# Performance work log

Measured on AMD Instinct MI355X. Metric: run time of the kernel, lower is better.

The kernel has to match this reference:

```python
import jax, jax.numpy as jnp
import numpy as np
import math

B, S, D = 16, 2048, 64


def setup_inputs() -> dict:
    key = jax.random.key(0)
    k1, k2, k3 = jax.random.split(key, 3)
    Q = jax.random.normal(k1, (B, S, D), dtype=jnp.float32)
    K = jax.random.normal(k2, (B, S, D), dtype=jnp.float32)
    V = jax.random.normal(k3, (B, S, D), dtype=jnp.float32)
    # causal mask: True where attention is disallowed (strict upper triangle)
    mask = jnp.triu(jnp.ones((S, S), dtype=bool), k=1)
    mask = jnp.broadcast_to(mask, (B, S, S))
    return {"Q": Q, "K": K, "V": V, "mask": mask, "dk": 64}


def reference(Q, K, V, mask, dk):
    # w = Q K^T / sqrt(dk), masked fill with -1e8
    w = jnp.einsum("bqd,bkd->bqk", Q, K) / math.sqrt(dk)
    w = jnp.where(mask, jnp.float32(-1.0e8), w)
    # distance_func in the original returns 0 (constant, under no_grad),
    # so exp(-1e8 * 0) * w == w; output is softmax of masked scaled scores.
    distance_score = jnp.float32(0.0)
    s = jnp.exp(jnp.float32(-1.0e8) * distance_score) * w
    a = jax.nn.softmax(s, axis=-1)
    return a
```

## Files before the change

kernel.cpp:

```cpp
#include <hip/hip_runtime.h>

using bf16x8 = __attribute__((ext_vector_type(8))) short;
using u16x8  = __attribute__((ext_vector_type(8))) unsigned short;
using f32x4  = __attribute__((ext_vector_type(4))) float;

static constexpr int S  = 2048;
static constexpr int D  = 64;
static constexpr int TQ = 64;
static constexpr float QSCALE = 0.18033688f;

__device__ __forceinline__ unsigned short bf16_rne(float x) {
    unsigned u = __builtin_bit_cast(unsigned, x);
    u += 0x7FFFu + ((u >> 16) & 1u);
    return (unsigned short)(u >> 16);
}
__device__ __forceinline__ f32x4 mfma16(bf16x8 a, bf16x8 b, f32x4 c) {
    return __builtin_amdgcn_mfma_f32_16x16x32_bf16(a, b, c, 0, 0, 0);
}
__device__ __forceinline__ void lbar() {
    asm volatile("s_waitcnt lgkmcnt(0)" ::: "memory");
    __builtin_amdgcn_s_barrier();
    asm volatile("" ::: "memory");
}

__global__ __launch_bounds__(512, 1)
void monotonic_attn(const float* __restrict__ Qg, const float* __restrict__ Kg,
                    float* __restrict__ out)
{
    __shared__ unsigned short qlds[4096];
    __shared__ unsigned short kls[8][2][1024];
    __shared__ float red[8][64];

    const int bid  = blockIdx.x;
    const int wid  = (bid & 7) * ((int)gridDim.x >> 3) + (bid >> 3);
    const int b    = wid >> 4;
    const int pair = wid & 15;

    const int tid = threadIdx.x, lane = tid & 63, wv = tid >> 6;
    const int l15 = lane & 15, g = lane >> 4;

    const float* __restrict__ Qb = Qg + (size_t)b * S * D;
    const float* __restrict__ Kb = Kg + (size_t)b * S * D;
    float* __restrict__ outb = out + (size_t)b * (size_t)S * S;

    const int srow  = lane >> 2;
    const int scp   = lane & 3;
    const int woff0 = srow * 64 + (((scp << 1)    ) ^ (srow & 7)) * 8;
    const int woff1 = srow * 64 + (((scp << 1) | 1) ^ (srow & 7)) * 8;
    const int roff0 = l15 * 64 + ((g    ) ^ (l15 & 7)) * 8;
    const int roff1 = l15 * 64 + ((4 | g) ^ (l15 & 7)) * 8;

    auto cidx = [&](int i) { return 2 * wv + ((i >> 1) << 4) + (i & 1); };

    for (int half = 0; half < 2; ++half) {
        const int qt   = half ? pair : 31 - pair;
        const int q0   = qt * TQ;
        const int kend = q0 + TQ;
        const int nC   = kend >> 4;
        const int ni   = (nC > 2 * wv) ? (((nC - 2 * wv + 15) >> 4) << 1) : 0;

        lbar();
        {
            const int qrow = tid >> 3, qcp = tid & 7;
            const float4* src = reinterpret_cast<const float4*>(Qb + (size_t)(q0 + qrow) * D + qcp * 8);
            const float4 f0 = src[0], f1 = src[1];
            float v[8];
            *reinterpret_cast<float4*>(&v[0]) = f0;
            *reinterpret_cast<float4*>(&v[4]) = f1;
            u16x8 hv;
            #pragma unroll
            for (int i = 0; i < 8; ++i) hv[i] = bf16_rne(v[i] * QSCALE);
            const int off = qrow * 64 + (qcp ^ (qrow & 7)) * 8;
            *reinterpret_cast<u16x8*>(&qlds[off]) = hv;
        }
        lbar();

        bf16x8 qf[4][2];
        #pragma unroll
        for (int qs = 0; qs < 4; ++qs) {
            const int row = qs * 16 + l15;
            #pragma unroll
            for (int c = 0; c < 2; ++c) {
                const int off = row * 64 + ((((c << 2) | g)) ^ (row & 7)) * 8;
                qf[qs][c] = *reinterpret_cast<const bf16x8*>(&qlds[off]);
            }
        }

        float inv4[4];
        for (int pass = 0; pass < 2; ++pass) {
            float rsum[4] = {0.f, 0.f, 0.f, 0.f};

            float4 ra0, ra1, ra2, ra3, rb0, rb1, rb2, rb3;
            auto issueA = [&](int i) {
                const float4* p4 = reinterpret_cast<const float4*>(Kb) + (cidx(i) << 8) + (lane << 2);
                ra0 = p4[0]; ra1 = p4[1]; ra2 = p4[2]; ra3 = p4[3];
            };
            auto issueB = [&](int i) {
                const float4* p4 = reinterpret_cast<const float4*>(Kb) + (cidx(i) << 8) + (lane << 2);
                rb0 = p4[0]; rb1 = p4[1]; rb2 = p4[2]; rb3 = p4[3];
            };
            auto stage = [&](int i, const float4& x0, const float4& x1,
                             const float4& x2, const float4& x3) {
                float v[16];
                *reinterpret_cast<float4*>(&v[0])  = x0;
                *reinterpret_cast<float4*>(&v[4])  = x1;
                *reinterpret_cast<float4*>(&v[8])  = x2;
                *reinterpret_cast<float4*>(&v[12]) = x3;
                u16x8 h0, h1;
                #pragma unroll
                for (int j = 0; j < 8; ++j) {
                    h0[j] = bf16_rne(v[j]);
                    h1[j] = bf16_rne(v[8 + j]);
                }
                unsigned short* bp = &kls[wv][i & 1][0];
                *reinterpret_cast<u16x8*>(&bp[woff0]) = h0;
                *reinterpret_cast<u16x8*>(&bp[woff1]) = h1;
            };
            auto comp = [&](int i) {
                const unsigned short* bp = &kls[wv][i & 1][0];
                const bf16x8 kf0 = *reinterpret_cast<const bf16x8*>(&bp[roff0]);
                const bf16x8 kf1 = *reinterpret_cast<const bf16x8*>(&bp[roff1]);
                const int klo = cidx(i) << 4;
                const int kb  = klo + g * 4;
                #pragma unroll
                for (int qs = 0; qs < 4; ++qs) {
                    const int qmin = q0 + qs * 16, qg = qmin + l15;
                    if (pass == 0) {
                        if (klo > qmin + 15) continue;
                        f32x4 acc = {0.f, 0.f, 0.f, 0.f};
                        acc = mfma16(kf0, qf[qs][0], acc);
                        acc = mfma16(kf1, qf[qs][1], acc);
                        if (klo + 15 <= qmin) {
                            rsum[qs] += exp2f(acc[0]) + exp2f(acc[1]) + exp2f(acc[2]) + exp2f(acc[3]);
                        } else {
                            #pragma unroll
                            for (int r = 0; r < 4; ++r)
                                rsum[qs] += (kb + r <= qg) ? exp2f(acc[r]) : 0.f;
                        }
                    } else {
                        f32x4 ov = {0.f, 0.f, 0.f, 0.f};
                        if (klo <= qmin + 15) {
                            f32x4 acc = {0.f, 0.f, 0.f, 0.f};
                            acc = mfma16(kf0, qf[qs][0], acc);
                            acc = mfma16(kf1, qf[qs][1], acc);
                            if (klo + 15 <= qmin) {
                                ov[0] = exp2f(acc[0]) * inv4[qs];
                                ov[1] = exp2f(acc[1]) * inv4[qs];
                                ov[2] = exp2f(acc[2]) * inv4[qs];
                                ov[3] = exp2f(acc[3]) * inv4[qs];
                            } else {
                                ov[0] = (kb + 0 <= qg) ? exp2f(acc[0]) * inv4[qs] : 0.f;
                                ov[1] = (kb + 1 <= qg) ? exp2f(acc[1]) * inv4[qs] : 0.f;
                                ov[2] = (kb + 2 <= qg) ? exp2f(acc[2]) * inv4[qs] : 0.f;
                                ov[3] = (kb + 3 <= qg) ? exp2f(acc[3]) * inv4[qs] : 0.f;
                            }
                        }
                        *reinterpret_cast<f32x4*>(outb + (size_t)qg * S + kb) = ov;
                    }
                }
            };

            if (ni > 0) issueA(0);
            if (ni > 1) issueB(1);
            int i = 0;
            for (; i + 2 <= ni; i += 2) {
                stage(i, ra0, ra1, ra2, ra3);
                if (i + 2 < ni) issueA(i + 2);
                comp(i);
                stage(i + 1, rb0, rb1, rb2, rb3);
                if (i + 3 < ni) issueB(i + 3);
                comp(i + 1);
            }
            if (i < ni) { stage(i, ra0, ra1, ra2, ra3); comp(i); }

            if (pass == 0) {
                #pragma unroll
                for (int qs = 0; qs < 4; ++qs) {
                    float v = rsum[qs];
                    v += __shfl_xor(v, 16);
                    v += __shfl_xor(v, 32);
                    if (g == 0) red[wv][qs * 16 + l15] = v;
                }
                lbar();
                #pragma unroll
                for (int qs = 0; qs < 4; ++qs) {
                    const int qi = qs * 16 + l15;
                    inv4[qs] = 1.f / (red[0][qi] + red[1][qi] + red[2][qi] + red[3][qi]
                                    + red[4][qi] + red[5][qi] + red[6][qi] + red[7][qi]);
                }
            }
        }

        {
            f32x4 z = {0.f, 0.f, 0.f, 0.f};
            const size_t rb = (size_t)(q0 + (tid >> 3)) * S;
            for (int cc = kend + (tid & 7) * 4; cc < S; cc += 32)
                *reinterpret_cast<f32x4*>(&outb[rb + cc]) = z;
        }
    }
}

extern "C" void kernel_launch(void* const* d_in, const int* in_sizes, int n_in,
                              void* d_out, int out_size, void* d_ws, size_t ws_size,
                              hipStream_t stream)
{
    const float* Q = (const float*)d_in[0];
    const float* K = (const float*)d_in[1];
    float* out     = (float*)d_out;
    const int nb   = in_sizes[0] / (S * D);

    monotonic_attn<<<dim3(nb * 16), dim3(512), 0, stream>>>(Q, K, out);
}
```

Before: 72.34 us.

## Split paired query tiles into separate 256-thread blocks with XCD-aware batch mapping

Each block now handles one 64-row query tile with 4 waves instead of two paired tiles with 8 waves, doubling the grid and allowing two blocks per CU. The block-to-batch mapping assigns two batches per XCD, ordering tiles longest-first so the causal triangle's uneven work spreads across the dispatch. The aim is finer-grained load balancing and better L2 locality of K per XCD. In exchange, the deliberate long/short pairing of tiles inside a block is dropped, and each wave now walks twice as many K chunks per tile.

```diff
diff --git a/kernel.cpp b/kernel.cpp
--- a/kernel.cpp
+++ b/kernel.cpp
@@ -23,18 +23,20 @@
     asm volatile("" ::: "memory");
 }
 
-__global__ __launch_bounds__(512, 1)
+__global__ __launch_bounds__(256, 2)
 void monotonic_attn(const float* __restrict__ Qg, const float* __restrict__ Kg,
                     float* __restrict__ out)
 {
     __shared__ unsigned short qlds[4096];
-    __shared__ unsigned short kls[8][2][1024];
-    __shared__ float red[8][64];
+    __shared__ unsigned short kls[4][2][1024];
+    __shared__ float red[4][64];
 
     const int bid  = blockIdx.x;
-    const int wid  = (bid & 7) * ((int)gridDim.x >> 3) + (bid >> 3);
-    const int b    = wid >> 4;
-    const int pair = wid & 15;
+    const int xcd  = bid & 7;
+    const int m    = bid >> 3;
+    const int bloc = (m < 32) ? 0 : 1;
+    const int qt   = (m < 32) ? (31 - m) : (m - 32);
+    const int b    = 2 * xcd + bloc;
 
     const int tid = threadIdx.x, lane = tid & 63, wv = tid >> 6;
     const int l15 = lane & 15, g = lane >> 4;
@@ -42,6 +44,11 @@
     const float* __restrict__ Qb = Qg + (size_t)b * S * D;
     const float* __restrict__ Kb = Kg + (size_t)b * S * D;
     float* __restrict__ outb = out + (size_t)b * (size_t)S * S;
+
+    const int q0   = qt * TQ;
+    const int kend = q0 + TQ;
+    const int nC   = kend >> 4;
+    const int ni   = (nC - wv + 3) >> 2;
 
     const int srow  = lane >> 2;
     const int scp   = lane & 3;
@@ -50,153 +57,146 @@
     const int roff0 = l15 * 64 + ((g    ) ^ (l15 & 7)) * 8;
     const int roff1 = l15 * 64 + ((4 | g) ^ (l15 & 7)) * 8;
 
-    auto cidx = [&](int i) { return 2 * wv + ((i >> 1) << 4) + (i & 1); };
-
-    for (int half = 0; half < 2; ++half) {
-        const int qt   = half ? pair : 31 - pair;
-        const int q0   = qt * TQ;
-        const int kend = q0 + TQ;
-        const int nC   = kend >> 4;
-        const int ni   = (nC > 2 * wv) ? (((nC - 2 * wv + 15) >> 4) << 1) : 0;
-
-        lbar();
-        {
-            const int qrow = tid >> 3, qcp = tid & 7;
-            const float4* src = reinterpret_cast<const float4*>(Qb + (size_t)(q0 + qrow) * D + qcp * 8);
-            const float4 f0 = src[0], f1 = src[1];
-            float v[8];
-            *reinterpret_cast<float4*>(&v[0]) = f0;
-            *reinterpret_cast<float4*>(&v[4]) = f1;
+    {
+        const int qrow = tid >> 2, qc = tid & 3;
+        const float4* src = reinterpret_cast<const float4*>(Qb + (size_t)(q0 + qrow) * D + qc * 16);
+        float v[16];
+        *reinterpret_cast<float4*>(&v[0])  = src[0];
+        *reinterpret_cast<float4*>(&v[4])  = src[1];
+        *reinterpret_cast<float4*>(&v[8])  = src[2];
+        *reinterpret_cast<float4*>(&v[12]) = src[3];
+        #pragma unroll
+        for (int j = 0; j < 2; ++j) {
             u16x8 hv;
             #pragma unroll
-            for (int i = 0; i < 8; ++i) hv[i] = bf16_rne(v[i] * QSCALE);
-            const int off = qrow * 64 + (qcp ^ (qrow & 7)) * 8;
+            for (int i = 0; i < 8; ++i) hv[i] = bf16_rne(v[8 * j + i] * QSCALE);
+            const int chunk = qc * 2 + j;
+            const int off = qrow * 64 + (chunk ^ (qrow & 7)) * 8;
             *reinterpret_cast<u16x8*>(&qlds[off]) = hv;
         }
-        lbar();
-
-        bf16x8 qf[4][2];
+    }
+    lbar();
+
+    bf16x8 qf[4][2];
+    #pragma unroll
+    for (int qs = 0; qs < 4; ++qs) {
+        const int row = qs * 16 + l15;
         #pragma unroll
-        for (int qs = 0; qs < 4; ++qs) {
-            const int row = qs * 16 + l15;
-            #pragma unroll
-            for (int c = 0; c < 2; ++c) {
-                const int off = row * 64 + ((((c << 2) | g)) ^ (row & 7)) * 8;
-                qf[qs][c] = *reinterpret_cast<const bf16x8*>(&qlds[off]);
-            }
-        }
-
-        float inv4[4];
-        for (int pass = 0; pass < 2; ++pass) {
-            float rsum[4] = {0.f, 0.f, 0.f, 0.f};
-
-            float4 ra0, ra1, ra2, ra3, rb0, rb1, rb2, rb3;
-            auto issueA = [&](int i) {
-                const float4* p4 = reinterpret_cast<const float4*>(Kb) + (cidx(i) << 8) + (lane << 2);
-                ra0 = p4[0]; ra1 = p4[1]; ra2 = p4[2]; ra3 = p4[3];
-            };
-            auto issueB = [&](int i) {
-                const float4* p4 = reinterpret_cast<const float4*>(Kb) + (cidx(i) << 8) + (lane << 2);
-                rb0 = p4[0]; rb1 = p4[1]; rb2 = p4[2]; rb3 = p4[3];
-            };
-            auto stage = [&](int i, const float4& x0, const float4& x1,
-                             const float4& x2, const float4& x3) {
-                float v[16];
-                *reinterpret_cast<float4*>(&v[0])  = x0;
-                *reinterpret_cast<float4*>(&v[4])  = x1;
-                *reinterpret_cast<float4*>(&v[8])  = x2;
-                *reinterpret_cast<float4*>(&v[12]) = x3;
-                u16x8 h0, h1;
-                #pragma unroll
-                for (int j = 0; j < 8; ++j) {
-                    h0[j] = bf16_rne(v[j]);
-                    h1[j] = bf16_rne(v[8 + j]);
-                }
-                unsigned short* bp = &kls[wv][i & 1][0];
-                *reinterpret_cast<u16x8*>(&bp[woff0]) = h0;
-                *reinterpret_cast<u16x8*>(&bp[woff1]) = h1;
-            };
-            auto comp = [&](int i) {
-                const unsigned short* bp = &kls[wv][i & 1][0];
-                const bf16x8 kf0 = *reinterpret_cast<const bf16x8*>(&bp[roff0]);
-                const bf16x8 kf1 = *reinterpret_cast<const bf16x8*>(&bp[roff1]);
-                const int klo = cidx(i) << 4;
-                const int kb  = klo + g * 4;
-                #pragma unroll
-                for (int qs = 0; qs < 4; ++qs) {
-                    const int qmin = q0 + qs * 16, qg = qmin + l15;
-                    if (pass == 0) {
-                        if (klo > qmin + 15) continue;
+        for (int c = 0; c < 2; ++c) {
+            const int off = row * 64 + ((((c << 2) | g)) ^ (row & 7)) * 8;
+            qf[qs][c] = *reinterpret_cast<const bf16x8*>(&qlds[off]);
+        }
+    }
+
+    float inv4[4];
+    for (int pass = 0; pass < 2; ++pass) {
+        float rsum[4] = {0.f, 0.f, 0.f, 0.f};
+
+        float4 ra0, ra1, ra2, ra3, rb0, rb1, rb2, rb3;
+        auto issueA = [&](int i) {
+            const float4* p4 = reinterpret_cast<const float4*>(Kb) + ((wv + 4 * i) << 8) + (lane << 2);
+            ra0 = p4[0]; ra1 = p4[1]; ra2 = p4[2]; ra3 = p4[3];
+        };
+        auto issueB = [&](int i) {
+            const float4* p4 = reinterpret_cast<const float4*>(Kb) + ((wv + 4 * i) << 8) + (lane << 2);
+            rb0 = p4[0]; rb1 = p4[1]; rb2 = p4[2]; rb3 = p4[3];
+        };
+        auto stage = [&](int i, const float4& x0, const float4& x1,
+                         const float4& x2, const float4& x3) {
+            float v[16];
+            *reinterpret_cast<float4*>(&v[0])  = x0;
+            *reinterpret_cast<float4*>(&v[4])  = x1;
+            *reinterpret_cast<float4*>(&v[8])  = x2;
+            *reinterpret_cast<float4*>(&v[12]) = x3;
+            u16x8 h0, h1;
+            #pragma unroll
+            for (int j = 0; j < 8; ++j) {
+                h0[j] = bf16_rne(v[j]);
+                h1[j] = bf16_rne(v[8 + j]);
+            }
+            unsigned short* bp = &kls[wv][i & 1][0];
+            *reinterpret_cast<u16x8*>(&bp[woff0]) = h0;
+            *reinterpret_cast<u16x8*>(&bp[woff1]) = h1;
+        };
+        auto comp = [&](int i) {
+            const unsigned short* bp = &kls[wv][i & 1][0];
+            const bf16x8 kf0 = *reinterpret_cast<const bf16x8*>(&bp[roff0]);
+            const bf16x8 kf1 = *reinterpret_cast<const bf16x8*>(&bp[roff1]);
+            const int klo = (wv + 4 * i) << 4;
+            const int kb  = klo + g * 4;
+            #pragma unroll
+            for (int qs = 0; qs < 4; ++qs) {
+                const int qmin = q0 + qs * 16, qg = qmin + l15;
+                if (pass == 0) {
+                    if (klo > qmin + 15) continue;
+                    f32x4 acc = {0.f, 0.f, 0.f, 0.f};
+                    acc = mfma16(kf0, qf[qs][0], acc);
+                    acc = mfma16(kf1, qf[qs][1], acc);
+                    if (klo + 15 <= qmin) {
+                        rsum[qs] += exp2f(acc[0]) + exp2f(acc[1]) + exp2f(acc[2]) + exp2f(acc[3]);
+                    } else {
+                        #pragma unroll
+                        for (int r = 0; r < 4; ++r)
+                            rsum[qs] += (kb + r <= qg) ? exp2f(acc[r]) : 0.f;
+                    }
+                } else {
+                    f32x4 ov = {0.f, 0.f, 0.f, 0.f};
+                    if (klo <= qmin + 15) {
                         f32x4 acc = {0.f, 0.f, 0.f, 0.f};
                         acc = mfma16(kf0, qf[qs][0], acc);
                         acc = mfma16(kf1, qf[qs][1], acc);
                         if (klo + 15 <= qmin) {
-                            rsum[qs] += exp2f(acc[0]) + exp2f(acc[1]) + exp2f(acc[2]) + exp2f(acc[3]);
+                            ov[0] = exp2f(acc[0]) * inv4[qs];
+                            ov[1] = exp2f(acc[1]) * inv4[qs];
+                            ov[2] = exp2f(acc[2]) * inv4[qs];
+                            ov[3] = exp2f(acc[3]) * inv4[qs];
                         } else {
-                            #pragma unroll
-                            for (int r = 0; r < 4; ++r)
-                                rsum[qs] += (kb + r <= qg) ? exp2f(acc[r]) : 0.f;
+                            ov[0] = (kb + 0 <= qg) ? exp2f(acc[0]) * inv4[qs] : 0.f;
+                            ov[1] = (kb + 1 <= qg) ? exp2f(acc[1]) * inv4[qs] : 0.f;
+                            ov[2] = (kb + 2 <= qg) ? exp2f(acc[2]) * inv4[qs] : 0.f;
+                            ov[3] = (kb + 3 <= qg) ? exp2f(acc[3]) * inv4[qs] : 0.f;
                         }
-                    } else {
-                        f32x4 ov = {0.f, 0.f, 0.f, 0.f};
-                        if (klo <= qmin + 15) {
-                            f32x4 acc = {0.f, 0.f, 0.f, 0.f};
-                            acc = mfma16(kf0, qf[qs][0], acc);
-                            acc = mfma16(kf1, qf[qs][1], acc);
-                            if (klo + 15 <= qmin) {
-                                ov[0] = exp2f(acc[0]) * inv4[qs];
-                                ov[1] = exp2f(acc[1]) * inv4[qs];
-                                ov[2] = exp2f(acc[2]) * inv4[qs];
-                                ov[3] = exp2f(acc[3]) * inv4[qs];
-                            } else {
-                                ov[0] = (kb + 0 <= qg) ? exp2f(acc[0]) * inv4[qs] : 0.f;
-                                ov[1] = (kb + 1 <= qg) ? exp2f(acc[1]) * inv4[qs] : 0.f;
-                                ov[2] = (kb + 2 <= qg) ? exp2f(acc[2]) * inv4[qs] : 0.f;
-                                ov[3] = (kb + 3 <= qg) ? exp2f(acc[3]) * inv4[qs] : 0.f;
-                            }
-                        }
-                        *reinterpret_cast<f32x4*>(outb + (size_t)qg * S + kb) = ov;
                     }
+                    *reinterpret_cast<f32x4*>(outb + (size_t)qg * S + kb) = ov;
                 }
-            };
-
-            if (ni > 0) issueA(0);
-            if (ni > 1) issueB(1);
-            int i = 0;
-            for (; i + 2 <= ni; i += 2) {
-                stage(i, ra0, ra1, ra2, ra3);
-                if (i + 2 < ni) issueA(i + 2);
-                comp(i);
-                stage(i + 1, rb0, rb1, rb2, rb3);
-                if (i + 3 < ni) issueB(i + 3);
-                comp(i + 1);
-            }
-            if (i < ni) { stage(i, ra0, ra1, ra2, ra3); comp(i); }
-
-            if (pass == 0) {
-                #pragma unroll
-                for (int qs = 0; qs < 4; ++qs) {
-                    float v = rsum[qs];
-                    v += __shfl_xor(v, 16);
-                    v += __shfl_xor(v, 32);
-                    if (g == 0) red[wv][qs * 16 + l15] = v;
-                }
-                lbar();
-                #pragma unroll
-                for (int qs = 0; qs < 4; ++qs) {
-                    const int qi = qs * 16 + l15;
-                    inv4[qs] = 1.f / (red[0][qi] + red[1][qi] + red[2][qi] + red[3][qi]
-                                    + red[4][qi] + red[5][qi] + red[6][qi] + red[7][qi]);
-                }
-            }
-        }
-
-        {
-            f32x4 z = {0.f, 0.f, 0.f, 0.f};
-            const size_t rb = (size_t)(q0 + (tid >> 3)) * S;
-            for (int cc = kend + (tid & 7) * 4; cc < S; cc += 32)
-                *reinterpret_cast<f32x4*>(&outb[rb + cc]) = z;
-        }
+            }
+        };
+
+        if (ni > 0) issueA(0);
+        if (ni > 1) issueB(1);
+        int i = 0;
+        for (; i + 2 <= ni; i += 2) {
+            stage(i, ra0, ra1, ra2, ra3);
+            if (i + 2 < ni) issueA(i + 2);
+            comp(i);
+            stage(i + 1, rb0, rb1, rb2, rb3);
+            if (i + 3 < ni) issueB(i + 3);
+            comp(i + 1);
+        }
+        if (i < ni) { stage(i, ra0, ra1, ra2, ra3); comp(i); }
+
+        if (pass == 0) {
+            #pragma unroll
+            for (int qs = 0; qs < 4; ++qs) {
+                float v = rsum[qs];
+                v += __shfl_xor(v, 16);
+                v += __shfl_xor(v, 32);
+                if (g == 0) red[wv][qs * 16 + l15] = v;
+            }
+            lbar();
+            #pragma unroll
+            for (int qs = 0; qs < 4; ++qs) {
+                const int qi = qs * 16 + l15;
+                inv4[qs] = 1.f / (red[0][qi] + red[1][qi] + red[2][qi] + red[3][qi]);
+            }
+        }
+    }
+
+    {
+        f32x4 z = {0.f, 0.f, 0.f, 0.f};
+        const size_t rb = (size_t)(q0 + (tid >> 2)) * S;
+        for (int cc = kend + (tid & 3) * 4; cc < S; cc += 16)
+            *reinterpret_cast<f32x4*>(&outb[rb + cc]) = z;
     }
 }
 
@@ -209,5 +209,5 @@
     float* out     = (float*)d_out;
     const int nb   = in_sizes[0] / (S * D);
 
-    monotonic_attn<<<dim3(nb * 16), dim3(512), 0, stream>>>(Q, K, out);
-}
+    monotonic_attn<<<dim3(nb * 32), dim3(256), 0, stream>>>(Q, K, out);
+}
```

Measured after the change: 64.52 us. 10.8% less time.
